# Optimization experiments

Measured on AMD Instinct MI355X. Metric: run time of the kernel, lower is better.

Reference implementation:

```python
import jax, jax.numpy as jnp
import numpy as np

N_HEAD = 16

def setup_inputs() -> dict:
    key = jax.random.key(0)
    k1, k2, k3 = jax.random.split(key, 3)
    B, T, C = 2, 2048, 1024
    x = jax.random.normal(k1, (B, T, C), dtype=jnp.float32)
    W_attn = jax.random.normal(k2, (C, 3 * C), dtype=jnp.float32) * (C ** -0.5)
    b_attn = jnp.zeros((3 * C,), dtype=jnp.float32)
    W_proj = jax.random.normal(k3, (C, C), dtype=jnp.float32) * (C ** -0.5)
    b_proj = jnp.zeros((C,), dtype=jnp.float32)
    return {"x": x, "W_attn": W_attn, "b_attn": b_attn, "W_proj": W_proj, "b_proj": b_proj}

def reference(x, W_attn, b_attn, W_proj, b_proj):
    B, T, C = x.shape
    H = N_HEAD
    D = C // H  # head_dim
    scale = D ** -0.5
    qkv = x @ W_attn + b_attn                       # [B,T,3C]
    q, k, v = jnp.split(qkv, 3, axis=-1)
    # [B,T,C] -> [B,H,T,D]
    q = q.reshape(B, T, H, D).transpose(0, 2, 1, 3)
    k = k.reshape(B, T, H, D).transpose(0, 2, 1, 3)
    v = v.reshape(B, T, H, D).transpose(0, 2, 1, 3)
    att = jnp.einsum('bhqd,bhkd->bhqk', q, k) * scale
    causal = jnp.tril(jnp.ones((T, T), dtype=bool))
    att = jnp.where(causal, att, jnp.float32(-jnp.inf))
    att = jax.nn.softmax(att, axis=-1)
    y = jnp.einsum('bhqk,bhkd->bhqd', att, v)       # [B,H,T,D]
    y = y.transpose(0, 2, 1, 3).reshape(B, T, C)
    return y @ W_proj + b_proj
```

## Files before the change

### kernel.cpp

```cpp
#include <hip/hip_runtime.h>

typedef __bf16 bf16;
typedef __bf16 bf16x4 __attribute__((ext_vector_type(4)));
typedef __bf16 bf16x8 __attribute__((ext_vector_type(8)));
typedef short s16x4 __attribute__((ext_vector_type(4)));
typedef float f32x4 __attribute__((ext_vector_type(4)));
typedef unsigned int u32x4 __attribute__((ext_vector_type(4)));

#define NB 2
#define NT 2048
#define NC 1024
#define NH 16
#define ND 64

#if __has_builtin(__builtin_amdgcn_exp2f)
#define EXP2F(x) __builtin_amdgcn_exp2f(x)
#else
#define EXP2F(x) __expf(0.69314718055994531f * (x))
#endif

#if __has_builtin(__builtin_amdgcn_rcpf)
#define RCPF(x) __builtin_amdgcn_rcpf(x)
#else
#define RCPF(x) (1.0f / (x))
#endif

__device__ __forceinline__ void async16(const void* g, void* l) {
  __builtin_amdgcn_global_load_lds(
      (const __attribute__((address_space(1))) void*)g,
      (__attribute__((address_space(3))) void*)l, 16, 0, 0);
}

__device__ __forceinline__ bf16x8 ld8(const bf16* p) {
  return *reinterpret_cast<const bf16x8*>(p);
}
__device__ __forceinline__ bf16x4 ld4(const bf16* p) {
  return *reinterpret_cast<const bf16x4*>(p);
}

__device__ __forceinline__ f32x4 mfma16(bf16x4 a, bf16x4 b, f32x4 c) {
  s16x4 ai = __builtin_bit_cast(s16x4, a);
  s16x4 bi = __builtin_bit_cast(s16x4, b);
#if __has_builtin(__builtin_amdgcn_mfma_f32_16x16x16bf16_1k)
  return __builtin_amdgcn_mfma_f32_16x16x16bf16_1k(ai, bi, c, 0, 0, 0);
#else
  f32x4 d;
  asm("v_mfma_f32_16x16x16_bf16 %0, %1, %2, %3"
      : "=v"(d) : "v"(ai), "v"(bi), "v"(c));
  return d;
#endif
}

__global__ __launch_bounds__(256) void prep(
    const float* __restrict__ x, bf16* __restrict__ xb,
    const float* __restrict__ Wa, bf16* __restrict__ Da,
    const float* __restrict__ Wp, bf16* __restrict__ Dp) {
  int bx = blockIdx.x;
  if (bx < 2048) {
    int i = (bx * 256 + threadIdx.x) * 8;
    const float4* s = (const float4*)(x + i);
    float4 a = s[0], b = s[1];
    bf16x8 o;
    o[0] = (bf16)a.x; o[1] = (bf16)a.y; o[2] = (bf16)a.z; o[3] = (bf16)a.w;
    o[4] = (bf16)b.x; o[5] = (bf16)b.y; o[6] = (bf16)b.z; o[7] = (bf16)b.w;
    *(bf16x8*)(xb + i) = o;
    return;
  }
  __shared__ float tile[32][33];
  int idx = bx - 2048;
  const float* src;
  bf16* dst;
  int Cc, cb, rb;
  if (idx < 96 * 32) { src = Wa; dst = Da; Cc = 3072; cb = idx % 96; rb = idx / 96; }
  else { idx -= 96 * 32; src = Wp; dst = Dp; Cc = 1024; cb = idx % 32; rb = idx / 32; }
  int tx = threadIdx.x & 31, ty = threadIdx.x >> 5;
  int r0 = rb * 32, c0 = cb * 32;
#pragma unroll
  for (int i = 0; i < 4; ++i)
    tile[ty + i * 8][tx] = src[(size_t)(r0 + ty + i * 8) * Cc + c0 + tx];
  __syncthreads();
#pragma unroll
  for (int i = 0; i < 4; ++i)
    dst[(size_t)(c0 + ty + i * 8) * 1024 + r0 + tx] = (bf16)tile[tx][ty + i * 8];
}

__global__ __launch_bounds__(256, 3) void gemm_qkv(
    const bf16* __restrict__ A,
    const bf16* __restrict__ Bt,
    const float* __restrict__ bias,
    bf16* __restrict__ Qo, bf16* __restrict__ Ko, bf16* __restrict__ Vto) {
  const int K = 1024;
  __shared__ bf16 As[128 * 32];
  __shared__ bf16 Bs[128 * 32];
  const int tid = threadIdx.x;
  const int lane = tid & 63, wv = tid >> 6;
  const int quad = lane >> 4, ln = lane & 15;
  const int m0 = blockIdx.x * 128, n0 = blockIdx.y * 128;
  const int wr = (wv >> 1) * 64, wc = (wv & 1) * 64;
  const int rA = tid >> 2, cA = (tid & 3) * 8;
  f32x4 acc[4][4] = {};

  for (int kt = 0; kt < K / 32; ++kt) {
    const int k0 = kt * 32;
#pragma unroll
    for (int inst = 0; inst < 2; ++inst) {
      async16(A + (size_t)(m0 + inst * 64 + rA) * K + k0 + cA,
              &As[inst * 2048 + wv * 512]);
      async16(Bt + (size_t)(n0 + inst * 64 + rA) * K + k0 + cA,
              &Bs[inst * 2048 + wv * 512]);
    }
    __syncthreads();
    bf16x8 aF[4], bF[4];
#pragma unroll
    for (int i = 0; i < 4; ++i) {
      aF[i] = ld8(&As[(wr + i * 16 + ln) * 32 + quad * 8]);
      bF[i] = ld8(&Bs[(wc + i * 16 + ln) * 32 + quad * 8]);
    }
#pragma unroll
    for (int rb = 0; rb < 4; ++rb)
#pragma unroll
      for (int cb = 0; cb < 4; ++cb)
        acc[rb][cb] = __builtin_amdgcn_mfma_f32_16x16x32_bf16(
            aF[rb], bF[cb], acc[rb][cb], 0, 0, 0);
    __syncthreads();
  }
#pragma unroll
  for (int rb = 0; rb < 4; ++rb) {
#pragma unroll
    for (int cb = 0; cb < 4; ++cb) {
      int gn = n0 + wc + cb * 16 + ln;
      int part = gn >> 10, c = gn & 1023;
      int h = c >> 6, dd = c & 63;
      float bs = bias[gn];
      int gm0 = m0 + wr + rb * 16 + quad * 4;
      int b = gm0 >> 11, t0 = gm0 & 2047;
      if (part == 2) {
        bf16x4 vv;
#pragma unroll
        for (int r = 0; r < 4; ++r) vv[r] = (bf16)(acc[rb][cb][r] + bs);
        *(bf16x4*)(Vto + ((size_t)(b * NH + h) * ND + dd) * NT + t0) = vv;
      } else {
        bf16* dst = part == 0 ? Qo : Ko;
        float sc = part == 0 ? 0.18033688f : 1.0f;
#pragma unroll
        for (int r = 0; r < 4; ++r)
          dst[((size_t)(b * NH + h) * NT + t0 + r) * ND + dd] =
              (bf16)((acc[rb][cb][r] + bs) * sc);
      }
    }
  }
}

__global__ __launch_bounds__(512, 4) void flash_attn_kernel(
    const bf16* __restrict__ Qg, const bf16* __restrict__ Kg,
    const bf16* __restrict__ Vtg, bf16* __restrict__ Yg) {
  __shared__ __align__(16) char smem[2][16384];
  const int tid = threadIdx.x;
  const int lane = tid & 63, wv = tid >> 6;
  const int quad = lane >> 4, ln = lane & 15;
  const int bid = blockIdx.x;
  const int qt = 15 - (bid >> 5);
  const int bh = bid & 31;
  const int bb = bh >> 4, hh = bh & 15;
  const int q0w = qt * 128 + wv * 16;
  const bf16* Qp = Qg + ((size_t)bh * NT + q0w) * ND;
  const bf16* Kbase = Kg + (size_t)bh * NT * ND;
  const bf16* Vtbase = Vtg + (size_t)bh * ND * NT;

  const int sub = lane >> 3, sch = lane & 7;
  const int swz = ln & 7;

  bf16x8 qf[2];
#pragma unroll
  for (int ks = 0; ks < 2; ++ks)
    qf[ks] = ld8(Qp + (size_t)ln * ND + ks * 32 + quad * 8);

  f32x4 oacc[4] = {};
  float li = 0.f;

  const int ktiles = 2 * qt + 2;
  const int cw = 2 * qt + 1 + (wv >> 2);

#define STAGE(KT, P)                                                           \
  {                                                                            \
    const int k0s = (KT) * 64;                                                 \
    char* Kl = smem[P];                                                        \
    char* Vl = smem[P] + 8192;                                                 \
    int row = wv * 8 + sub;                                                    \
    int gch = sch ^ sub;                                                       \
    async16(Kbase + (size_t)(k0s + row) * ND + gch * 8, Kl + wv * 8 * 128);    \
    async16(Vtbase + (size_t)row * NT + k0s + gch * 8, Vl + wv * 8 * 128);     \
  }

  STAGE(0, 0);
  for (int kt = 0; kt < ktiles; ++kt) {
    const int p = kt & 1;
    __syncthreads();
    if (kt + 1 < ktiles) STAGE(kt + 1, p ^ 1);
    if (kt < cw) {
      const char* Kl = smem[p];
      const char* Vl = smem[p] + 8192;
      const int k0 = kt * 64;
      f32x4 sacc[4] = {};
#pragma unroll
      for (int ks = 0; ks < 2; ++ks) {
        bf16x8 kfr[4];
#pragma unroll
        for (int cb = 0; cb < 4; ++cb)
          kfr[cb] = *(const bf16x8*)(Kl + (cb * 16 + ln) * 128 +
                                     (((ks * 4 + quad) ^ swz) * 16));
#pragma unroll
        for (int cb = 0; cb < 4; ++cb)
          sacc[cb] = __builtin_amdgcn_mfma_f32_16x16x32_bf16(
              kfr[cb], qf[ks], sacc[cb], 0, 0, 0);
      }
      if (k0 + 63 > q0w) {
        int qr = q0w + ln;
#pragma unroll
        for (int cb = 0; cb < 4; ++cb)
#pragma unroll
          for (int r = 0; r < 4; ++r) {
            int kc = k0 + cb * 16 + quad * 4 + r;
            if (kc > qr) sacc[cb][r] = -1e30f;
          }
      }
      bf16x4 pf[4];
      float rs = 0.f;
#pragma unroll
      for (int cb = 0; cb < 4; ++cb) {
        bf16x4 pv;
#pragma unroll
        for (int r = 0; r < 4; ++r) {
          float pexp = EXP2F(sacc[cb][r]);
          rs += pexp;
          pv[r] = (bf16)pexp;
        }
        pf[cb] = pv;
      }
      li += rs;
#pragma unroll
      for (int cb = 0; cb < 4; ++cb) {
        bf16x4 vfr[4];
#pragma unroll
        for (int db = 0; db < 4; ++db)
          vfr[db] = *(const bf16x4*)(Vl + (db * 16 + ln) * 128 +
                                     (((cb * 2 + (quad >> 1)) ^ swz) * 16) +
                                     (quad & 1) * 8);
#pragma unroll
        for (int db = 0; db < 4; ++db)
          oacc[db] = mfma16(vfr[db], pf[cb], oacc[db]);
      }
    }
  }
#undef STAGE

  li += __shfl_xor(li, 16);
  li += __shfl_xor(li, 32);

  float inv = RCPF(li);
  int row = q0w + ln;
#pragma unroll
  for (int db = 0; db < 4; ++db) {
    bf16x4 ov;
#pragma unroll
    for (int r = 0; r < 4; ++r) ov[r] = (bf16)(oacc[db][r] * inv);
    *(bf16x4*)(Yg + ((size_t)(bb * NT + row)) * NC + hh * 64 + db * 16 +
               quad * 4) = ov;
  }
}

__global__ __launch_bounds__(256, 2) void gemm_proj(
    const bf16* __restrict__ A,
    const bf16* __restrict__ Bt,
    const float* __restrict__ bias,
    float* __restrict__ out) {
  const int K = 1024;
  __shared__ bf16 As[128 * 32];
  __shared__ bf16 Bs[64 * 32];
  const int tid = threadIdx.x;
  const int lane = tid & 63, wv = tid >> 6;
  const int quad = lane >> 4, ln = lane & 15;
  const int m0 = blockIdx.x * 128, n0 = blockIdx.y * 64;
  const int wr = wv * 32;
  const int rA = tid >> 2, cA = (tid & 3) * 8;
  f32x4 acc[2][4] = {};

  for (int kt = 0; kt < K / 32; ++kt) {
    const int k0 = kt * 32;
#pragma unroll
    for (int inst = 0; inst < 2; ++inst)
      async16(A + (size_t)(m0 + inst * 64 + rA) * K + k0 + cA,
              &As[inst * 2048 + wv * 512]);
    async16(Bt + (size_t)(n0 + rA) * K + k0 + cA, &Bs[wv * 512]);
    __syncthreads();
    bf16x8 aF[2], bF[4];
#pragma unroll
    for (int i = 0; i < 2; ++i)
      aF[i] = ld8(&As[(wr + i * 16 + ln) * 32 + quad * 8]);
#pragma unroll
    for (int i = 0; i < 4; ++i)
      bF[i] = ld8(&Bs[(i * 16 + ln) * 32 + quad * 8]);
#pragma unroll
    for (int rb = 0; rb < 2; ++rb)
#pragma unroll
      for (int cb = 0; cb < 4; ++cb)
        acc[rb][cb] = __builtin_amdgcn_mfma_f32_16x16x32_bf16(
            aF[rb], bF[cb], acc[rb][cb], 0, 0, 0);
    __syncthreads();
  }
#pragma unroll
  for (int rb = 0; rb < 2; ++rb) {
#pragma unroll
    for (int cb = 0; cb < 4; ++cb) {
      int gn = n0 + cb * 16 + ln;
      float bs = bias[gn];
#pragma unroll
      for (int r = 0; r < 4; ++r) {
        int gm = m0 + wr + rb * 16 + quad * 4 + r;
        out[(size_t)gm * 1024 + gn] = acc[rb][cb][r] + bs;
      }
    }
  }
}

extern "C" void kernel_launch(void* const* d_in, const int* in_sizes, int n_in,
                              void* d_out, int out_size, void* d_ws, size_t ws_size,
                              hipStream_t stream) {
  const float* x      = (const float*)d_in[0];
  const float* W_attn = (const float*)d_in[1];
  const float* b_attn = (const float*)d_in[2];
  const float* W_proj = (const float*)d_in[3];
  const float* b_proj = (const float*)d_in[4];
  float* out = (float*)d_out;

  bf16* ws  = (bf16*)d_ws;
  bf16* xb  = ws;
  bf16* Wab = xb + (size_t)4096 * 1024;
  bf16* Wpb = Wab + (size_t)3072 * 1024;
  bf16* Qb  = Wpb + (size_t)1024 * 1024;
  bf16* Kb  = Qb + (size_t)32 * 2048 * 64;
  bf16* Vtb = Kb + (size_t)32 * 2048 * 64;
  bf16* Yb  = xb;

  prep<<<2048 + 96 * 32 + 32 * 32, 256, 0, stream>>>(x, xb, W_attn, Wab,
                                                     W_proj, Wpb);
  gemm_qkv<<<dim3(32, 24), 256, 0, stream>>>(xb, Wab, b_attn, Qb, Kb, Vtb);
  flash_attn_kernel<<<512, 512, 0, stream>>>(Qb, Kb, Vtb, Yb);
  gemm_proj<<<dim3(32, 16), 256, 0, stream>>>(Yb, Wpb, b_proj, out);
}
```

Baseline: 169.7 us.

## Use 128-key tiles in flash attention and reorder query-tile scheduling

Widens the K/V shared-memory tile from 64 to 128 keys per iteration, which halves the number of loop iterations and barriers and doubles the MFMA work done per synchronization. The swizzle for the 256-byte V rows is changed to match. The per-wave causal skip is removed, so each wave processes every tile up to the diagonal and masks only the last one, which adds some wasted compute for lower waves. Block order also changes: heavy query tiles were dispatched first and light ones now go first. Doubled LDS (64KB per block) may reduce occupancy below the launch-bounds target.

```diff
diff --git a/kernel.cpp b/kernel.cpp
--- a/kernel.cpp
+++ b/kernel.cpp
@@ -154,12 +154,12 @@
 __global__ __launch_bounds__(512, 4) void flash_attn_kernel(
     const bf16* __restrict__ Qg, const bf16* __restrict__ Kg,
     const bf16* __restrict__ Vtg, bf16* __restrict__ Yg) {
-  __shared__ __align__(16) char smem[2][16384];
+  __shared__ __align__(16) char smem[2][32768];
   const int tid = threadIdx.x;
   const int lane = tid & 63, wv = tid >> 6;
   const int quad = lane >> 4, ln = lane & 15;
   const int bid = blockIdx.x;
-  const int qt = 15 - (bid >> 5);
+  const int qt = bid >> 5;
   const int bh = bid & 31;
   const int bb = bh >> 4, hh = bh & 15;
   const int q0w = qt * 128 + wv * 16;
@@ -167,7 +167,8 @@
   const bf16* Kbase = Kg + (size_t)bh * NT * ND;
   const bf16* Vtbase = Vtg + (size_t)bh * ND * NT;
 
-  const int sub = lane >> 3, sch = lane & 7;
+  const int sub8 = lane >> 3, sch8 = lane & 7;
+  const int sub16 = lane >> 4, sch16 = lane & 15;
   const int swz = ln & 7;
 
   bf16x8 qf[2];
@@ -178,18 +179,25 @@
   f32x4 oacc[4] = {};
   float li = 0.f;
 
-  const int ktiles = 2 * qt + 2;
-  const int cw = 2 * qt + 1 + (wv >> 2);
+  const int ktiles = qt + 1;
 
 #define STAGE(KT, P)                                                           \
   {                                                                            \
-    const int k0s = (KT) * 64;                                                 \
+    const int k0s = (KT) * 128;                                                \
     char* Kl = smem[P];                                                        \
-    char* Vl = smem[P] + 8192;                                                 \
-    int row = wv * 8 + sub;                                                    \
-    int gch = sch ^ sub;                                                       \
-    async16(Kbase + (size_t)(k0s + row) * ND + gch * 8, Kl + wv * 8 * 128);    \
-    async16(Vtbase + (size_t)row * NT + k0s + gch * 8, Vl + wv * 8 * 128);     \
+    char* Vl = smem[P] + 16384;                                                \
+    _Pragma("unroll") for (int i = 0; i < 2; ++i) {                            \
+      int r0 = wv * 16 + i * 8;                                                \
+      int row = r0 + sub8;                                                     \
+      int gch = sch8 ^ (row & 7);                                              \
+      async16(Kbase + (size_t)(k0s + row) * ND + gch * 8, Kl + r0 * 128);      \
+    }                                                                          \
+    _Pragma("unroll") for (int i = 0; i < 2; ++i) {                            \
+      int r0 = wv * 8 + i * 4;                                                 \
+      int row = r0 + sub16;                                                    \
+      int gch = sch16 ^ (row & 15);                                            \
+      async16(Vtbase + (size_t)row * NT + k0s + gch * 8, Vl + r0 * 256);       \
+    }                                                                          \
   }
 
   STAGE(0, 0);
@@ -197,59 +205,57 @@
     const int p = kt & 1;
     __syncthreads();
     if (kt + 1 < ktiles) STAGE(kt + 1, p ^ 1);
-    if (kt < cw) {
-      const char* Kl = smem[p];
-      const char* Vl = smem[p] + 8192;
-      const int k0 = kt * 64;
-      f32x4 sacc[4] = {};
-#pragma unroll
-      for (int ks = 0; ks < 2; ++ks) {
-        bf16x8 kfr[4];
-#pragma unroll
-        for (int cb = 0; cb < 4; ++cb)
-          kfr[cb] = *(const bf16x8*)(Kl + (cb * 16 + ln) * 128 +
-                                     (((ks * 4 + quad) ^ swz) * 16));
-#pragma unroll
-        for (int cb = 0; cb < 4; ++cb)
-          sacc[cb] = __builtin_amdgcn_mfma_f32_16x16x32_bf16(
-              kfr[cb], qf[ks], sacc[cb], 0, 0, 0);
+    const char* Kl = smem[p];
+    const char* Vl = smem[p] + 16384;
+    const int k0 = kt * 128;
+    f32x4 sacc[8] = {};
+#pragma unroll
+    for (int ks = 0; ks < 2; ++ks) {
+      bf16x8 kfr[8];
+#pragma unroll
+      for (int cb = 0; cb < 8; ++cb)
+        kfr[cb] = *(const bf16x8*)(Kl + (cb * 16 + ln) * 128 +
+                                   (((ks * 4 + quad) ^ swz) * 16));
+#pragma unroll
+      for (int cb = 0; cb < 8; ++cb)
+        sacc[cb] = __builtin_amdgcn_mfma_f32_16x16x32_bf16(
+            kfr[cb], qf[ks], sacc[cb], 0, 0, 0);
+    }
+    if (kt == qt) {
+      int qr = q0w + ln;
+#pragma unroll
+      for (int cb = 0; cb < 8; ++cb)
+#pragma unroll
+        for (int r = 0; r < 4; ++r) {
+          int kc = k0 + cb * 16 + quad * 4 + r;
+          if (kc > qr) sacc[cb][r] = -1e30f;
+        }
+    }
+    bf16x4 pf[8];
+    float rs = 0.f;
+#pragma unroll
+    for (int cb = 0; cb < 8; ++cb) {
+      bf16x4 pv;
+#pragma unroll
+      for (int r = 0; r < 4; ++r) {
+        float pexp = EXP2F(sacc[cb][r]);
+        rs += pexp;
+        pv[r] = (bf16)pexp;
       }
-      if (k0 + 63 > q0w) {
-        int qr = q0w + ln;
-#pragma unroll
-        for (int cb = 0; cb < 4; ++cb)
-#pragma unroll
-          for (int r = 0; r < 4; ++r) {
-            int kc = k0 + cb * 16 + quad * 4 + r;
-            if (kc > qr) sacc[cb][r] = -1e30f;
-          }
-      }
-      bf16x4 pf[4];
-      float rs = 0.f;
-#pragma unroll
-      for (int cb = 0; cb < 4; ++cb) {
-        bf16x4 pv;
-#pragma unroll
-        for (int r = 0; r < 4; ++r) {
-          float pexp = EXP2F(sacc[cb][r]);
-          rs += pexp;
-          pv[r] = (bf16)pexp;
-        }
-        pf[cb] = pv;
-      }
-      li += rs;
-#pragma unroll
-      for (int cb = 0; cb < 4; ++cb) {
-        bf16x4 vfr[4];
-#pragma unroll
-        for (int db = 0; db < 4; ++db)
-          vfr[db] = *(const bf16x4*)(Vl + (db * 16 + ln) * 128 +
-                                     (((cb * 2 + (quad >> 1)) ^ swz) * 16) +
-                                     (quad & 1) * 8);
-#pragma unroll
-        for (int db = 0; db < 4; ++db)
-          oacc[db] = mfma16(vfr[db], pf[cb], oacc[db]);
-      }
+      pf[cb] = pv;
+    }
+    li += rs;
+#pragma unroll
+    for (int cb = 0; cb < 8; ++cb) {
+      bf16x4 vfr[4];
+#pragma unroll
+      for (int db = 0; db < 4; ++db)
+        vfr[db] = *(const bf16x4*)(Vl + (db * 16 + ln) * 256 +
+                                   (((cb * 2 + (quad >> 1)) ^ ln) * 16) +
+                                   (quad & 1) * 8);
+#pragma unroll
+      for (int db = 0; db < 4; ++db)
+        oacc[db] = mfma16(vfr[db], pf[cb], oacc[db]);
     }
   }
 #undef STAGE
```

New measurement: 173.9 us. 1.03x slower.
